# Kernel optimization log

Hardware: AMD Instinct MI355X
Metric: run time of the kernel (lower is better)

## Reference

```python
import jax, jax.numpy as jnp
import numpy as np

HIDDEN = 256
B, L = 4, 4096


def setup_inputs() -> dict:
    key = jax.random.key(0)
    k_in, k_q, k_k, k_v, k_len = jax.random.split(key, 5)
    inputs = jax.random.normal(k_in, (B, L, HIDDEN), dtype=jnp.float32)
    # torch.rand -> uniform [0,1)
    W_query = jax.random.uniform(k_q, (HIDDEN, HIDDEN), dtype=jnp.float32)
    W_key = jax.random.uniform(k_k, (HIDDEN, HIDDEN), dtype=jnp.float32)
    W_value = jax.random.uniform(k_v, (HIDDEN, HIDDEN), dtype=jnp.float32)
    lengths = jax.random.randint(k_len, (B,), 1, L + 1, dtype=jnp.int64)
    return {"inputs": inputs, "W_query": W_query, "W_key": W_key,
            "W_value": W_value, "lengths": lengths}


def reference(inputs, W_query, W_key, W_value, lengths):
    # lengths is unused by the original module (no masking applied).
    # QKV projections (batched matmul with shared weight)
    queries = jnp.einsum('blh,hd->bld', inputs, W_query)
    keys = jnp.einsum('blh,hd->bld', inputs, W_key)
    values = jnp.einsum('blh,hd->bld', inputs, W_value)
    # scaled dot-product attention, full [B, L, L] scores as in original
    scale = 1.0 / jnp.sqrt(jnp.asarray(HIDDEN, dtype=inputs.dtype))
    attn_scores = jnp.einsum('bqd,bkd->bqk', queries, keys) * scale
    attentions = jax.nn.softmax(attn_scores, axis=-1)
    weighted = jnp.einsum('bqk,bkd->bqd', attentions, values)
    return weighted
```

## Files before the change

kernel.cpp:

```cpp
#include <hip/hip_runtime.h>


typedef __bf16 bf16x8 __attribute__((ext_vector_type(8)));
typedef _Float16 f16x8 __attribute__((ext_vector_type(8)));
typedef _Float16 f16x4 __attribute__((ext_vector_type(4)));
typedef float floatx4 __attribute__((ext_vector_type(4)));

#define MFMA16B(a, b, c) __builtin_amdgcn_mfma_f32_16x16x32_bf16(a, b, c, 0, 0, 0)
#define MFMA16F(a, b, c) __builtin_amdgcn_mfma_f32_16x16x32_f16(a, b, c, 0, 0, 0)
#define GLOAD_LDS16(g, l)                                                  \
  __builtin_amdgcn_global_load_lds(                                        \
      (const __attribute__((address_space(1))) void *)(g),                 \
      (__attribute__((address_space(3))) void *)(l), 16, 0, 0)

#define HID 256
#define LSEQ 4096
#define NB 4
#define NTOK (NB * LSEQ)
#define PLANE ((size_t)NTOK * HID)
#define QSCALE 0.09016844005556021f


__device__ __forceinline__ void split_bf16(float v, __bf16 &h, __bf16 &l) {
  h = (__bf16)v;
  l = (__bf16)(v - (float)h);
}

template <int N>
__device__ __forceinline__ float dpp_ror(float v) {
  return __builtin_bit_cast(float,
      __builtin_amdgcn_update_dpp(0, __builtin_bit_cast(int, v),
                                  0x120 + N, 0xf, 0xf, true));
}
__device__ __forceinline__ float row_sum16(float v) {
  v += dpp_ror<1>(v);
  v += dpp_ror<2>(v);
  v += dpp_ror<4>(v);
  v += dpp_ror<8>(v);
  return v;
}
__device__ __forceinline__ float row_max16(float v) {
  v = fmaxf(v, dpp_ror<1>(v));
  v = fmaxf(v, dpp_ror<2>(v));
  v = fmaxf(v, dpp_ror<4>(v));
  v = fmaxf(v, dpp_ror<8>(v));
  return v;
}

__global__ __launch_bounds__(256) void wsplit(const float *__restrict__ Wq,
                                              const float *__restrict__ Wk,
                                              const float *__restrict__ Wv,
                                              __bf16 *__restrict__ Wht,
                                              __bf16 *__restrict__ Wlt) {
  __shared__ float tile[32][256];
  const int wsel = blockIdx.x;
  const int hb = blockIdx.y;
  const float *W = (wsel == 0) ? Wq : (wsel == 1) ? Wk : Wv;
  __bf16 *oh = Wht + wsel * HID * HID;
  __bf16 *ol = Wlt + wsel * HID * HID;
  const int t = threadIdx.x;
  #pragma unroll
  for (int p = 0; p < 8; ++p) {
    int r = p * 4 + (t >> 6);
    int c = (t & 63) * 4;
    *(floatx4 *)&tile[r][c] = *(const floatx4 *)&W[(hb * 32 + r) * HID + c];
  }
  __syncthreads();
  #pragma unroll
  for (int q = 0; q < 4; ++q) {
    int n = q * 64 + (t >> 2);
    int hs = (t & 3) * 8;
    bf16x8 hh, ll;
    #pragma unroll
    for (int i = 0; i < 8; ++i) {
      float v = tile[hs + i][n];
      __bf16 h, l;
      split_bf16(v, h, l);
      hh[i] = h; ll[i] = l;
    }
    *(bf16x8 *)&oh[n * HID + hb * 32 + hs] = hh;
    *(bf16x8 *)&ol[n * HID + hb * 32 + hs] = ll;
  }
}

__global__ __launch_bounds__(256, 2) void qkv_proj(const float *__restrict__ X,
                                                   const __bf16 *__restrict__ Wht,
                                                   const __bf16 *__restrict__ Wlt,
                                                   _Float16 *__restrict__ Qf,
                                                   _Float16 *__restrict__ Kf,
                                                   _Float16 *__restrict__ Vf) {
  __shared__ __bf16 WhS[64 * 256];
  __shared__ __bf16 WlS[64 * 256];
  _Float16 *Tf = (_Float16 *)WhS;

  const int mtile = blockIdx.x;
  const int col0 = blockIdx.y * 64;
  const int tid = threadIdx.x;
  const int w4 = tid >> 6;
  const int lane = tid & 63;
  const int quad = lane >> 4;
  const int ln = lane & 15;
  const int arow = mtile * 64 + w4 * 16 + ln;

  bf16x8 ah[8], al[8];
  #pragma unroll
  for (int kc = 0; kc < 8; ++kc) {
    const float *xp = X + (size_t)arow * HID + kc * 32 + quad * 8;
    floatx4 x0 = *(const floatx4 *)xp;
    floatx4 x1 = *(const floatx4 *)(xp + 4);
    #pragma unroll
    for (int j = 0; j < 4; ++j) {
      __bf16 h, l;
      split_bf16(x0[j], h, l); ah[kc][j] = h; al[kc][j] = l;
      split_bf16(x1[j], h, l); ah[kc][4 + j] = h; al[kc][4 + j] = l;
    }
  }

  const int srow = tid >> 2;
  const int sseg = tid & 3;

  bf16x8 pwh[8], pwl[8];
  {
    const size_t wbase = (size_t)(col0 + srow) * HID;
    #pragma unroll
    for (int j = 0; j < 8; ++j) {
      const int chunk = j * 4 + sseg;
      pwh[j] = *(const bf16x8 *)&Wht[wbase + chunk * 8];
      pwl[j] = *(const bf16x8 *)&Wlt[wbase + chunk * 8];
    }
  }

  for (int w = 0; w < 3; ++w) {
    __syncthreads();
    #pragma unroll
    for (int j = 0; j < 8; ++j) {
      const int chunk = j * 4 + sseg;
      const int dst = srow * 256 + ((chunk ^ (srow & 7)) << 3);
      *(bf16x8 *)&WhS[dst] = pwh[j];
      *(bf16x8 *)&WlS[dst] = pwl[j];
    }
    __syncthreads();

    if (w < 2) {
      const size_t wbase = (size_t)(w + 1) * HID * HID + (size_t)(col0 + srow) * HID;
      #pragma unroll
      for (int j = 0; j < 8; ++j) {
        const int chunk = j * 4 + sseg;
        pwh[j] = *(const bf16x8 *)&Wht[wbase + chunk * 8];
        pwl[j] = *(const bf16x8 *)&Wlt[wbase + chunk * 8];
      }
    }

    floatx4 acc[4] = {};
    #pragma unroll
    for (int kc = 0; kc < 8; ++kc) {
      #pragma unroll
      for (int nt = 0; nt < 4; ++nt) {
        const int a = (nt * 16 + ln) * 256 + (((kc * 4 + quad) ^ (ln & 7)) << 3);
        bf16x8 bh = *(const bf16x8 *)&WhS[a];
        bf16x8 bl = *(const bf16x8 *)&WlS[a];
        acc[nt] = MFMA16B(ah[kc], bh, acc[nt]);
        acc[nt] = MFMA16B(ah[kc], bl, acc[nt]);
        acc[nt] = MFMA16B(al[kc], bh, acc[nt]);
      }
    }

    if (w == 0) {
      #pragma unroll
      for (int nt = 0; nt < 4; ++nt) {
        #pragma unroll
        for (int r = 0; r < 4; ++r) {
          const int orow = mtile * 64 + w4 * 16 + quad * 4 + r;
          const int ocol = col0 + nt * 16 + ln;
          Qf[(size_t)orow * HID + ocol] = (_Float16)(acc[nt][r] * QSCALE);
        }
      }
    } else if (w == 1) {
      __syncthreads();
      #pragma unroll
      for (int nt = 0; nt < 4; ++nt) {
        #pragma unroll
        for (int r = 0; r < 4; ++r) {
          const int tok_l = w4 * 16 + quad * 4 + r;
          const int h_l = nt * 16 + ln;
          Tf[tok_l * 72 + h_l] = (_Float16)acc[nt][r];
        }
      }
      __syncthreads();
      #pragma unroll
      for (int i = 0; i < 2; ++i) {
        const int c = i * 256 + tid;
        const int lane_f = c & 63;
        const int ntf = (c >> 6) & 1;
        const int kcL = (c >> 7) & 1;
        const int t2 = (c >> 8) & 1;
        const int qf = lane_f >> 4;
        const int lnf = lane_f & 15;
        const int tok_l = t2 * 32 + ntf * 16 + lnf;
        f16x8 v = *(const f16x8 *)&Tf[tok_l * 72 + kcL * 32 + qf * 8];
        const int T = mtile * 2 + t2;
        const int kc = (col0 >> 5) + kcL;
        *(f16x8 *)&Kf[(size_t)T * 8192 + ((ntf * 8 + kc) * 64 + lane_f) * 8] = v;
      }
    } else {
      __syncthreads();
      #pragma unroll
      for (int nt = 0; nt < 4; ++nt) {
        #pragma unroll
        for (int r = 0; r < 4; ++r) {
          const int tok_l = w4 * 16 + quad * 4 + r;
          const int d_l = nt * 16 + ln;
          Tf[d_l * 72 + tok_l] = (_Float16)acc[nt][r];
        }
      }
      __syncthreads();
      #pragma unroll
      for (int i = 0; i < 2; ++i) {
        const int c = i * 256 + tid;
        const int lane_f = c & 63;
        const int dtL = (c >> 6) & 3;
        const int t2 = (c >> 8) & 1;
        const int qf = lane_f >> 4;
        const int lnf = lane_f & 15;
        const int d_l = dtL * 16 + lnf;
        f16x8 v = *(const f16x8 *)&Tf[d_l * 72 + t2 * 32 + qf * 8];
        const int T = mtile * 2 + t2;
        const int dt = (col0 >> 4) + dtL;
        *(f16x8 *)&Vf[(size_t)(T * 16 + dt) * 512 + lane_f * 8] = v;
      }
    }
  }
}

__global__ __launch_bounds__(256, 2) void attn(const _Float16 *__restrict__ Qf,
                                               const _Float16 *__restrict__ Kf,
                                               const _Float16 *__restrict__ Vf,
                                               _Float16 *__restrict__ Op,
                                               float *__restrict__ Mp,
                                               float *__restrict__ Lp) {
  __shared__ _Float16 KS0[8192];
  __shared__ _Float16 KS1[8192];
  __shared__ _Float16 PsS[4 * 16 * 72];

  const int bx = blockIdx.x;
  const int ks = bx & 1;
  const int qt = bx >> 1;
  const int b = qt >> 6;
  const int qtl = qt & 63;
  const int tid = threadIdx.x;
  const int w4 = tid >> 6;
  const int lane = tid & 63;
  const int quad = lane >> 4;
  const int ln = lane & 15;
  const int T0 = b * 128 + ks * 64;

  const int qtok = b * LSEQ + qtl * 64 + w4 * 16 + ln;
  f16x8 q[8];
  #pragma unroll
  for (int kc = 0; kc < 8; ++kc)
    q[kc] = *(const f16x8 *)&Qf[(size_t)qtok * HID + kc * 32 + quad * 8];

  const _Float16 *kuni = Kf + (size_t)T0 * 8192;
  const _Float16 *vuni = Vf + (size_t)T0 * 8192;
  const int koff = tid * 8;
  const int voff = lane * 8;

  #pragma unroll
  for (int i = 0; i < 4; ++i)
    GLOAD_LDS16(kuni + i * 2048 + koff, &KS0[i * 2048 + koff]);

  float m[4] = {-1e30f, -1e30f, -1e30f, -1e30f};
  float l[4] = {0.f, 0.f, 0.f, 0.f};
  floatx4 o[16] = {};

  for (int jm = 0; jm < 32; ++jm) {
    floatx4 s[4];
    __syncthreads();
    {
      const _Float16 *src = kuni + (size_t)(2 * jm + 1) * 8192 + koff;
      #pragma unroll
      for (int i = 0; i < 4; ++i)
        GLOAD_LDS16(src + i * 2048, &KS1[i * 2048 + koff]);
    }
    {
      floatx4 pa[2] = {}, pb[2] = {};
      #pragma unroll
      for (int nt = 0; nt < 2; ++nt)
        #pragma unroll
        for (int kc = 0; kc < 4; ++kc) {
          pa[nt] = MFMA16F(q[kc], *(const f16x8 *)(KS0 + (nt * 8 + kc) * 512 + voff), pa[nt]);
          pb[nt] = MFMA16F(q[4 + kc], *(const f16x8 *)(KS0 + (nt * 8 + 4 + kc) * 512 + voff), pb[nt]);
        }
      s[0] = pa[0] + pb[0];
      s[1] = pa[1] + pb[1];
    }
    __syncthreads();
    if (jm < 31) {
      const _Float16 *src = kuni + (size_t)(2 * jm + 2) * 8192 + koff;
      #pragma unroll
      for (int i = 0; i < 4; ++i)
        GLOAD_LDS16(src + i * 2048, &KS0[i * 2048 + koff]);
    }
    const _Float16 *va = vuni + (size_t)(2 * jm) * 8192;
    const _Float16 *vbp = vuni + (size_t)(2 * jm + 1) * 8192;
    f16x8 vb0[8];
    #pragma unroll
    for (int dt = 0; dt < 8; ++dt)
      vb0[dt] = *(const f16x8 *)(va + dt * 512 + voff);
    {
      floatx4 pa[2] = {}, pb[2] = {};
      #pragma unroll
      for (int nt = 0; nt < 2; ++nt)
        #pragma unroll
        for (int kc = 0; kc < 4; ++kc) {
          pa[nt] = MFMA16F(q[kc], *(const f16x8 *)(KS1 + (nt * 8 + kc) * 512 + voff), pa[nt]);
          pb[nt] = MFMA16F(q[4 + kc], *(const f16x8 *)(KS1 + (nt * 8 + 4 + kc) * 512 + voff), pb[nt]);
        }
      s[2] = pa[0] + pb[0];
      s[3] = pa[1] + pb[1];
    }
    f16x8 vb1[8];
    #pragma unroll
    for (int dt = 0; dt < 8; ++dt)
      vb1[dt] = *(const f16x8 *)(va + (8 + dt) * 512 + voff);

    float alpha[4];
    #pragma unroll
    for (int r = 0; r < 4; ++r) {
      const float tmax = row_max16(
          fmaxf(fmaxf(s[0][r], s[1][r]), fmaxf(s[2][r], s[3][r])));
      const float mn = fmaxf(m[r], tmax);
      const float al = exp2f(m[r] - mn);
      const float p0 = exp2f(s[0][r] - mn);
      const float p1 = exp2f(s[1][r] - mn);
      const float p2 = exp2f(s[2][r] - mn);
      const float p3 = exp2f(s[3][r] - mn);
      s[0][r] = p0; s[1][r] = p1; s[2][r] = p2; s[3][r] = p3;
      const float rs = row_sum16((p0 + p1) + (p2 + p3));
      l[r] = l[r] * al + rs;
      m[r] = mn;
      alpha[r] = al;
    }

    _Float16 *ps = PsS + w4 * 16 * 72;
    #pragma unroll
    for (int nt = 0; nt < 4; ++nt)
      #pragma unroll
      for (int r = 0; r < 4; ++r)
        ps[(quad * 4 + r) * 72 + nt * 16 + ln] = (_Float16)s[nt][r];

    const float amin = fminf(fminf(alpha[0], alpha[1]), fminf(alpha[2], alpha[3]));
    if (__any(amin < 1.0f)) {
      #pragma unroll
      for (int dt = 0; dt < 16; ++dt) {
        o[dt][0] *= alpha[0]; o[dt][1] *= alpha[1];
        o[dt][2] *= alpha[2]; o[dt][3] *= alpha[3];
      }
    }

    const f16x8 paA = *(const f16x8 *)&ps[ln * 72 + quad * 8];
    const f16x8 paB = *(const f16x8 *)&ps[ln * 72 + 32 + quad * 8];

    #pragma unroll
    for (int dt = 0; dt < 8; ++dt) o[dt] = MFMA16F(paA, vb0[dt], o[dt]);
    f16x8 vb2[8];
    #pragma unroll
    for (int dt = 0; dt < 8; ++dt)
      vb2[dt] = *(const f16x8 *)(vbp + dt * 512 + voff);
    #pragma unroll
    for (int dt = 0; dt < 8; ++dt) o[8 + dt] = MFMA16F(paA, vb1[dt], o[8 + dt]);
    f16x8 vb3[8];
    #pragma unroll
    for (int dt = 0; dt < 8; ++dt)
      vb3[dt] = *(const f16x8 *)(vbp + (8 + dt) * 512 + voff);
    #pragma unroll
    for (int dt = 0; dt < 8; ++dt) o[dt] = MFMA16F(paB, vb2[dt], o[dt]);
    #pragma unroll
    for (int dt = 0; dt < 8; ++dt) o[8 + dt] = MFMA16F(paB, vb3[dt], o[8 + dt]);
  }

  const int rowbase = b * LSEQ + qtl * 64 + w4 * 16 + quad * 4;
  #pragma unroll
  for (int dt = 0; dt < 16; ++dt)
    #pragma unroll
    for (int r = 0; r < 4; ++r)
      Op[(size_t)ks * PLANE + (size_t)(rowbase + r) * HID + dt * 16 + ln] =
          (_Float16)o[dt][r];
  if (ln == 0) {
    #pragma unroll
    for (int r = 0; r < 4; ++r) {
      Mp[ks * NTOK + rowbase + r] = m[r];
      Lp[ks * NTOK + rowbase + r] = l[r];
    }
  }
}

__global__ __launch_bounds__(256) void merge(const _Float16 *__restrict__ Op,
                                             const float *__restrict__ Mp,
                                             const float *__restrict__ Lp,
                                             float *__restrict__ Out) {
  const int row = blockIdx.x * 4 + (threadIdx.x >> 6);
  const int c = (threadIdx.x & 63) * 4;
  const float m0 = Mp[row], m1 = Mp[NTOK + row];
  const float l0 = Lp[row], l1 = Lp[NTOK + row];
  const float M = fmaxf(m0, m1);
  const float e0 = exp2f(m0 - M), e1 = exp2f(m1 - M);
  const float invL = 1.0f / (l0 * e0 + l1 * e1);
  const float w0 = e0 * invL, w1 = e1 * invL;
  f16x4 a = *(const f16x4 *)&Op[(size_t)row * HID + c];
  f16x4 b4 = *(const f16x4 *)&Op[PLANE + (size_t)row * HID + c];
  floatx4 out;
  #pragma unroll
  for (int i = 0; i < 4; ++i) out[i] = w0 * (float)a[i] + w1 * (float)b4[i];
  *(floatx4 *)&Out[(size_t)row * HID + c] = out;
}

extern "C" void kernel_launch(void *const *d_in, const int *in_sizes, int n_in,
                              void *d_out, int out_size, void *d_ws, size_t ws_size,
                              hipStream_t stream) {
  const float *X = (const float *)d_in[0];
  const float *Wq = (const float *)d_in[1];
  const float *Wk = (const float *)d_in[2];
  const float *Wv = (const float *)d_in[3];

  _Float16 *ws = (_Float16 *)d_ws;
  _Float16 *Qf = ws;
  _Float16 *Kf = Qf + PLANE;
  _Float16 *Vf = Kf + PLANE;
  __bf16 *Wht = (__bf16 *)(Vf + PLANE);
  __bf16 *Wlt = Wht + 3 * HID * HID;
  _Float16 *Op = (_Float16 *)(Wlt + 3 * HID * HID);
  float *Mp = (float *)(Op + 2 * PLANE);
  float *Lp = Mp + 2 * NTOK;

  wsplit<<<dim3(3, 8), 256, 0, stream>>>(Wq, Wk, Wv, Wht, Wlt);
  qkv_proj<<<dim3(256, 4), 256, 0, stream>>>(X, Wht, Wlt, Qf, Kf, Vf);
  attn<<<512, 256, 0, stream>>>(Qf, Kf, Vf, Op, Mp, Lp);
  merge<<<NTOK / 4, 256, 0, stream>>>(Op, Mp, Lp, (float *)d_out);
}
```

Measured before the change: 234.4 us.

## Split attention KV range four ways and raise occupancy with MFMA priority hints

The attention kernel now splits each query tile's key range into four chunks instead of two, launching twice as many blocks and asking for four blocks per CU instead of two. The P staging buffer is halved, reusing one 16x32 tile per half, and s_setprio brackets the MFMA sections so matrix work gets issue priority. The merge kernel combines four partial outputs. The aim is better CU saturation and latency hiding, at the cost of more partial-output traffic in merge, tighter register limits, and an extra LDS round trip per iteration.

```diff
diff --git a/kernel.cpp b/kernel.cpp
--- a/kernel.cpp
+++ b/kernel.cpp
@@ -18,6 +18,7 @@
 #define NB 4
 #define NTOK (NB * LSEQ)
 #define PLANE ((size_t)NTOK * HID)
+#define NSPLIT 4
 #define QSCALE 0.09016844005556021f
 
 
@@ -232,7 +233,7 @@
   }
 }
 
-__global__ __launch_bounds__(256, 2) void attn(const _Float16 *__restrict__ Qf,
+__global__ __launch_bounds__(256, 4) void attn(const _Float16 *__restrict__ Qf,
                                                const _Float16 *__restrict__ Kf,
                                                const _Float16 *__restrict__ Vf,
                                                _Float16 *__restrict__ Op,
@@ -240,11 +241,11 @@
                                                float *__restrict__ Lp) {
   __shared__ _Float16 KS0[8192];
   __shared__ _Float16 KS1[8192];
-  __shared__ _Float16 PsS[4 * 16 * 72];
+  __shared__ _Float16 PsS[4 * 16 * 40];
 
   const int bx = blockIdx.x;
-  const int ks = bx & 1;
-  const int qt = bx >> 1;
+  const int ks = bx & 3;
+  const int qt = bx >> 2;
   const int b = qt >> 6;
   const int qtl = qt & 63;
   const int tid = threadIdx.x;
@@ -252,7 +253,7 @@
   const int lane = tid & 63;
   const int quad = lane >> 4;
   const int ln = lane & 15;
-  const int T0 = b * 128 + ks * 64;
+  const int T0 = b * 128 + ks * 32;
 
   const int qtok = b * LSEQ + qtl * 64 + w4 * 16 + ln;
   f16x8 q[8];
@@ -273,7 +274,7 @@
   float l[4] = {0.f, 0.f, 0.f, 0.f};
   floatx4 o[16] = {};
 
-  for (int jm = 0; jm < 32; ++jm) {
+  for (int jm = 0; jm < 16; ++jm) {
     floatx4 s[4];
     __syncthreads();
     {
@@ -284,6 +285,7 @@
     }
     {
       floatx4 pa[2] = {}, pb[2] = {};
+      __builtin_amdgcn_s_setprio(1);
       #pragma unroll
       for (int nt = 0; nt < 2; ++nt)
         #pragma unroll
@@ -291,11 +293,12 @@
           pa[nt] = MFMA16F(q[kc], *(const f16x8 *)(KS0 + (nt * 8 + kc) * 512 + voff), pa[nt]);
           pb[nt] = MFMA16F(q[4 + kc], *(const f16x8 *)(KS0 + (nt * 8 + 4 + kc) * 512 + voff), pb[nt]);
         }
+      __builtin_amdgcn_s_setprio(0);
       s[0] = pa[0] + pb[0];
       s[1] = pa[1] + pb[1];
     }
     __syncthreads();
-    if (jm < 31) {
+    if (jm < 15) {
       const _Float16 *src = kuni + (size_t)(2 * jm + 2) * 8192 + koff;
       #pragma unroll
       for (int i = 0; i < 4; ++i)
@@ -309,6 +312,7 @@
       vb0[dt] = *(const f16x8 *)(va + dt * 512 + voff);
     {
       floatx4 pa[2] = {}, pb[2] = {};
+      __builtin_amdgcn_s_setprio(1);
       #pragma unroll
       for (int nt = 0; nt < 2; ++nt)
         #pragma unroll
@@ -316,6 +320,7 @@
           pa[nt] = MFMA16F(q[kc], *(const f16x8 *)(KS1 + (nt * 8 + kc) * 512 + voff), pa[nt]);
           pb[nt] = MFMA16F(q[4 + kc], *(const f16x8 *)(KS1 + (nt * 8 + 4 + kc) * 512 + voff), pb[nt]);
         }
+      __builtin_amdgcn_s_setprio(0);
       s[2] = pa[0] + pb[0];
       s[3] = pa[1] + pb[1];
     }
@@ -342,12 +347,12 @@
       alpha[r] = al;
     }
 
-    _Float16 *ps = PsS + w4 * 16 * 72;
-    #pragma unroll
-    for (int nt = 0; nt < 4; ++nt)
+    _Float16 *ps = PsS + w4 * (16 * 40);
+    #pragma unroll
+    for (int nt = 0; nt < 2; ++nt)
       #pragma unroll
       for (int r = 0; r < 4; ++r)
-        ps[(quad * 4 + r) * 72 + nt * 16 + ln] = (_Float16)s[nt][r];
+        ps[(quad * 4 + r) * 40 + nt * 16 + ln] = (_Float16)s[nt][r];
 
     const float amin = fminf(fminf(alpha[0], alpha[1]), fminf(alpha[2], alpha[3]));
     if (__any(amin < 1.0f)) {
@@ -358,25 +363,39 @@
       }
     }
 
-    const f16x8 paA = *(const f16x8 *)&ps[ln * 72 + quad * 8];
-    const f16x8 paB = *(const f16x8 *)&ps[ln * 72 + 32 + quad * 8];
-
+    const f16x8 paA = *(const f16x8 *)&ps[ln * 40 + quad * 8];
+
+    __builtin_amdgcn_s_setprio(1);
     #pragma unroll
     for (int dt = 0; dt < 8; ++dt) o[dt] = MFMA16F(paA, vb0[dt], o[dt]);
+    __builtin_amdgcn_s_setprio(0);
     f16x8 vb2[8];
     #pragma unroll
     for (int dt = 0; dt < 8; ++dt)
       vb2[dt] = *(const f16x8 *)(vbp + dt * 512 + voff);
+    __builtin_amdgcn_s_setprio(1);
     #pragma unroll
     for (int dt = 0; dt < 8; ++dt) o[8 + dt] = MFMA16F(paA, vb1[dt], o[8 + dt]);
+    __builtin_amdgcn_s_setprio(0);
     f16x8 vb3[8];
     #pragma unroll
     for (int dt = 0; dt < 8; ++dt)
       vb3[dt] = *(const f16x8 *)(vbp + (8 + dt) * 512 + voff);
+
+    #pragma unroll
+    for (int nt = 0; nt < 2; ++nt)
+      #pragma unroll
+      for (int r = 0; r < 4; ++r)
+        ps[(quad * 4 + r) * 40 + nt * 16 + ln] = (_Float16)s[2 + nt][r];
+
+    const f16x8 paB = *(const f16x8 *)&ps[ln * 40 + quad * 8];
+
+    __builtin_amdgcn_s_setprio(1);
     #pragma unroll
     for (int dt = 0; dt < 8; ++dt) o[dt] = MFMA16F(paB, vb2[dt], o[dt]);
     #pragma unroll
     for (int dt = 0; dt < 8; ++dt) o[8 + dt] = MFMA16F(paB, vb3[dt], o[8 + dt]);
+    __builtin_amdgcn_s_setprio(0);
   }
 
   const int rowbase = b * LSEQ + qtl * 64 + w4 * 16 + quad * 4;
@@ -401,17 +420,28 @@
                                              float *__restrict__ Out) {
   const int row = blockIdx.x * 4 + (threadIdx.x >> 6);
   const int c = (threadIdx.x & 63) * 4;
-  const float m0 = Mp[row], m1 = Mp[NTOK + row];
-  const float l0 = Lp[row], l1 = Lp[NTOK + row];
-  const float M = fmaxf(m0, m1);
-  const float e0 = exp2f(m0 - M), e1 = exp2f(m1 - M);
-  const float invL = 1.0f / (l0 * e0 + l1 * e1);
-  const float w0 = e0 * invL, w1 = e1 * invL;
-  f16x4 a = *(const f16x4 *)&Op[(size_t)row * HID + c];
-  f16x4 b4 = *(const f16x4 *)&Op[PLANE + (size_t)row * HID + c];
-  floatx4 out;
-  #pragma unroll
-  for (int i = 0; i < 4; ++i) out[i] = w0 * (float)a[i] + w1 * (float)b4[i];
+  float ms[NSPLIT], ls[NSPLIT];
+  #pragma unroll
+  for (int s = 0; s < NSPLIT; ++s) {
+    ms[s] = Mp[s * NTOK + row];
+    ls[s] = Lp[s * NTOK + row];
+  }
+  const float M = fmaxf(fmaxf(ms[0], ms[1]), fmaxf(ms[2], ms[3]));
+  float e[NSPLIT], den = 0.f;
+  #pragma unroll
+  for (int s = 0; s < NSPLIT; ++s) {
+    e[s] = exp2f(ms[s] - M);
+    den += ls[s] * e[s];
+  }
+  const float inv = 1.0f / den;
+  floatx4 out = {};
+  #pragma unroll
+  for (int s = 0; s < NSPLIT; ++s) {
+    const f16x4 a = *(const f16x4 *)&Op[(size_t)s * PLANE + (size_t)row * HID + c];
+    const float w = e[s] * inv;
+    #pragma unroll
+    for (int i = 0; i < 4; ++i) out[i] += w * (float)a[i];
+  }
   *(floatx4 *)&Out[(size_t)row * HID + c] = out;
 }
 
@@ -430,11 +460,11 @@
   __bf16 *Wht = (__bf16 *)(Vf + PLANE);
   __bf16 *Wlt = Wht + 3 * HID * HID;
   _Float16 *Op = (_Float16 *)(Wlt + 3 * HID * HID);
-  float *Mp = (float *)(Op + 2 * PLANE);
-  float *Lp = Mp + 2 * NTOK;
+  float *Mp = (float *)(Op + NSPLIT * PLANE);
+  float *Lp = Mp + NSPLIT * NTOK;
 
   wsplit<<<dim3(3, 8), 256, 0, stream>>>(Wq, Wk, Wv, Wht, Wlt);
   qkv_proj<<<dim3(256, 4), 256, 0, stream>>>(X, Wht, Wlt, Qf, Kf, Vf);
-  attn<<<512, 256, 0, stream>>>(Qf, Kf, Vf, Op, Mp, Lp);
+  attn<<<NTOK / 64 * NSPLIT, 256, 0, stream>>>(Qf, Kf, Vf, Op, Mp, Lp);
   merge<<<NTOK / 4, 256, 0, stream>>>(Op, Mp, Lp, (float *)d_out);
 }
```

Result: slower. 656.1 us (+179.9%).
